# Kernel tuning notes

Measured on AMD Instinct MI355X. Metric: run time of the kernel, lower is better.

The kernel has to match this reference:

```python
import jax, jax.numpy as jnp
import numpy as np

B, L, G, P, K = 16, 2048, 8, 8, 64
CLAMP = 15.0


def _cdist(x, y):
    # Euclidean pairwise distance: x [..., K, 3], y [..., L, 3] -> [..., K, L]
    x2 = jnp.sum(x * x, axis=-1)[..., :, None]
    y2 = jnp.sum(y * y, axis=-1)[..., None, :]
    xy = jnp.einsum('...kc,...lc->...kl', x, y)
    return jnp.sqrt(jnp.maximum(x2 + y2 - 2.0 * xy, 0.0))


def setup_inputs() -> dict:
    key = jax.random.key(0)
    k1, k2, k3 = jax.random.split(key, 3)
    rng = np.random.default_rng(0)
    # each group: K distinct atom indices; each of the P rows is a permutation of them
    auto = np.empty((G, P, K), dtype=np.int64)
    for g in range(G):
        base = rng.permutation(L)[:K]
        auto[g, 0] = base
        for j in range(1, P):
            auto[g, j] = base[rng.permutation(K)]
    return {
        'x_pred': jax.random.normal(k1, (B, L, 3), jnp.float32),
        'x_native': jax.random.normal(k2, (B, L, 3), jnp.float32),
        'x_native_mask': jax.random.randint(k3, (B, L), 0, 2).astype(bool),
        'automorphs': jnp.asarray(auto),
    }


def reference(x_pred, x_native, x_native_mask, automorphs):
    Bn, Ln = x_pred.shape[0], x_pred.shape[1]
    Kn = automorphs.shape[-1]
    batch_idx = jnp.arange(Bn)
    denom = jnp.asarray(Kn * (Ln - Kn), x_pred.dtype)

    def step(carry, a):
        x_nat, nat_mask = carry
        a0 = a[0]                                           # [K]
        # columns NOT in the symmetry group (the ~mask columns)
        colmask = jnp.ones((Ln,), x_pred.dtype).at[a0].set(0.0)
        d_pred = _cdist(x_pred[:, a0], x_pred)              # [B,K,L]
        gath = x_nat[:, a]                                  # [B,P,K,3]
        d_nat = _cdist(gath, x_nat[:, None])                # [B,P,K,L]
        drms = jnp.minimum(jnp.nan_to_num(jnp.square(d_pred[:, None] - d_nat)), CLAMP)
        drms = jnp.sum(drms * colmask, axis=(-1, -2)) / denom   # [B,P] masked mean
        bestj = jnp.argmin(drms, axis=1)                    # first min <=> strict-< update
        sel = gath[batch_idx, bestj]                        # [B,K,3]
        sel_m = nat_mask[:, a][batch_idx, bestj]            # [B,K]
        x_nat = x_nat.at[:, a0].set(sel)
        nat_mask = nat_mask.at[:, a0].set(sel_m)
        return (x_nat, nat_mask), None

    (x_nat, nat_mask), _ = jax.lax.scan(step, (x_native, x_native_mask), automorphs)
    return x_nat, nat_mask
```

## Files before the change

### kernel.cpp

```cpp
#include <hip/hip_runtime.h>
#include <math.h>

#define Bn 16
#define Ln 2048
#define Gn 8
#define Pn 8
#define Kn 64
#define CLAMP_V 15.0f

#define BPB 32
#define NTH 512
#define NWV (NTH / 64)
#define LPB (Ln / BPB)
#define LPW (LPB / NWV)
#define PK  (Pn * Kn)

#define MAGIC(g) (0x5EED0000u | (unsigned)(g))

typedef unsigned long long ull;

__device__ __forceinline__ float wave_sum64(float x) {
#define DPP_ADD(ctrl) \
    x += __int_as_float(__builtin_amdgcn_update_dpp(0, __float_as_int(x), ctrl, 0xf, 0xf, true))
    DPP_ADD(0x111);
    DPP_ADD(0x112);
    DPP_ADD(0x114);
    DPP_ADD(0x118);
    DPP_ADD(0x142);
    DPP_ADD(0x143);
#undef DPP_ADD
    return x;
}

template <int IMM>
__device__ __forceinline__ float swz_xor(float v) {
    return v + __int_as_float(__builtin_amdgcn_ds_swizzle(__float_as_int(v), IMM));
}
__device__ __forceinline__ ull ld_rlx64(const ull* p) {
    return __hip_atomic_load(p, __ATOMIC_RELAXED, __HIP_MEMORY_SCOPE_AGENT);
}
__device__ __forceinline__ void st_rlx64(ull* p, ull v) {
    __hip_atomic_store(p, v, __ATOMIC_RELAXED, __HIP_MEMORY_SCOPE_AGENT);
}

__global__ __launch_bounds__(NTH, 2) void fused_kernel(
    const float* __restrict__ xpred, const float* __restrict__ xnat,
    const int* __restrict__ mask_in, const int* __restrict__ autom,
    float* __restrict__ out_x, float* __restrict__ out_m,
    ull* __restrict__ part) {

    const int tid  = threadIdx.x;
    const int lane = tid & 63;
    const int wv   = tid >> 6;
    const int b    = blockIdx.x >> 5;
    const int c    = blockIdx.x & (BPB - 1);

    __shared__ float4         s_all[Ln];
    __shared__ unsigned short s_idx[Ln];
    __shared__ unsigned char  s_inv[2][Ln];
    __shared__ float4         s_xp[LPB];
    __shared__ float          s_part[NWV][Pn];

    const float* xpb = xpred + (size_t)b * Ln * 3;
    const float* xnb = xnat  + (size_t)b * Ln * 3;

    for (int l = tid; l < Ln; l += NTH) {
        s_idx[l] = (unsigned short)l;
        s_all[l] = make_float4(xnb[l * 3 + 0], xnb[l * 3 + 1], xnb[l * 3 + 2], 0.0f);
    }
    if (wv == 0) {
        const int l = c * LPB + lane;
        s_xp[lane] = make_float4(xpb[l * 3 + 0], xpb[l * 3 + 1], xpb[l * 3 + 2], 0.0f);
    } else if (wv == 2) {
        s_inv[0][autom[lane]] = (unsigned char)lane;
    }
    int   a0k = autom[lane];
    float px = xpb[a0k * 3 + 0], py = xpb[a0k * 3 + 1], pz = xpb[a0k * 3 + 2];
    __syncthreads();

    #pragma unroll 1
    for (int g = 0; g < Gn; g++) {
        const int* ag  = autom + g * PK;
        const int* ag1 = autom + (g + 1) * PK;
        const int  cur = g & 1, nxt = cur ^ 1;
        ull* pg = part + (size_t)(g * Bn + b) * (BPB * Pn);

        const float4 nk = s_all[s_idx[a0k]];
        int sig[Pn];
        #pragma unroll
        for (int p = 0; p < Pn; p++)
            sig[p] = 4 * (int)s_inv[cur][ag[p * Kn + lane]];
        unsigned short jl[LPW];
        #pragma unroll
        for (int i = 0; i < LPW; i++)
            jl[i] = s_idx[c * LPB + wv * LPW + i];

        float acc[Pn];
        #pragma unroll
        for (int p = 0; p < Pn; p++) acc[p] = 0.0f;

        #pragma unroll 2
        for (int i = 0; i < LPW; i++) {
            const int il = wv * LPW + i;
            const int l  = c * LPB + il;
            if (__ballot(a0k == l)) continue;

            const float4 q = s_xp[il];
            const float4 m = s_all[jl[i]];
            const float dx = px - q.x, dy = py - q.y, dz = pz - q.z;
            const float dp = __builtin_amdgcn_sqrtf(dx * dx + dy * dy + dz * dz);
            const float ex = nk.x - m.x, ey = nk.y - m.y, ez = nk.z - m.z;
            const float dn = __builtin_amdgcn_sqrtf(ex * ex + ey * ey + ez * ez);

            #pragma unroll
            for (int p = 0; p < Pn; p++) {
                const float dns = __int_as_float(
                    __builtin_amdgcn_ds_bpermute(sig[p], __float_as_int(dn)));
                const float e = dp - dns;
                acc[p] += fminf(e * e, CLAMP_V);
            }
        }

        #pragma unroll
        for (int p = 0; p < Pn; p++) {
            const float v = wave_sum64(acc[p]);
            if (lane == 63) s_part[wv][p] = v;
        }
        __syncthreads();

        if (wv == 0) {
            float v = s_part[lane >> 3][lane & 7];
            v = swz_xor<0x201F>(v);
            v = swz_xor<0x401F>(v);
            v += __shfl(v, lane + 32, 64);
            if (lane < 8)
                st_rlx64(&pg[c * Pn + lane],
                         ((ull)MAGIC(g) << 32) | (ull)__float_as_uint(v));
        }

        if (g < Gn - 1) {
            a0k = ag1[lane];
            px = xpb[a0k * 3 + 0]; py = xpb[a0k * 3 + 1]; pz = xpb[a0k * 3 + 2];
            if (wv == 2) s_inv[nxt][ag1[lane]] = (unsigned char)lane;
        }

        if (wv == 0) {
            const unsigned magic = MAGIC(g);
            ull q0 = 0, q1 = 0, q2 = 0, q3 = 0;
            bool r0 = false, r1 = false, r2 = false, r3 = false;
            for (;;) {
                if (!r0) { q0 = ld_rlx64(pg + lane);       r0 = (unsigned)(q0 >> 32) == magic; }
                if (!r1) { q1 = ld_rlx64(pg + lane + 64);  r1 = (unsigned)(q1 >> 32) == magic; }
                if (!r2) { q2 = ld_rlx64(pg + lane + 128); r2 = (unsigned)(q2 >> 32) == magic; }
                if (!r3) { q3 = ld_rlx64(pg + lane + 192); r3 = (unsigned)(q3 >> 32) == magic; }
                if (__ballot(!(r0 && r1 && r2 && r3)) == 0ull) break;
                __builtin_amdgcn_s_sleep(1);
            }
            float v = __uint_as_float((unsigned)q0) + __uint_as_float((unsigned)q1)
                    + __uint_as_float((unsigned)q2) + __uint_as_float((unsigned)q3);
            v = swz_xor<0x201F>(v);
            v = swz_xor<0x401F>(v);
            v += __shfl(v, lane + 32, 64);
            float best = __shfl(v, 0, 64);
            int   bj   = 0;
            #pragma unroll
            for (int p = 1; p < Pn; p++) {
                const float t = __shfl(v, p, 64);
                if (t < best) { best = t; bj = p; }
            }
            const unsigned short oldv = s_idx[ag[bj * Kn + lane]];
            s_idx[ag[lane]] = oldv;
        }
        __syncthreads();
    }

    const int l0 = c * LPB;
    if (tid < LPB * 3) {
        const int ll = tid / 3, coord = tid % 3;
        const int l  = l0 + ll;
        const float4 v = s_all[s_idx[l]];
        out_x[((size_t)b * Ln + l) * 3 + coord] =
            (coord == 0) ? v.x : ((coord == 1) ? v.y : v.z);
    } else if (tid < LPB * 4) {
        const int l = l0 + (tid - LPB * 3);
        const int j = s_idx[l];
        out_m[(size_t)b * Ln + l] = (float)mask_in[(size_t)b * Ln + j];
    }
}

extern "C" void kernel_launch(void* const* d_in, const int* in_sizes, int n_in,
                              void* d_out, int out_size, void* d_ws, size_t ws_size,
                              hipStream_t stream) {
    const float* xpred   = (const float*)d_in[0];
    const float* xnat_in = (const float*)d_in[1];
    const int*   mask_in = (const int*)  d_in[2];
    const int*   autom   = (const int*)  d_in[3];

    float* out_x = (float*)d_out;
    float* out_m = out_x + Bn * Ln * 3;

    ull* part = (ull*)d_ws;

    fused_kernel<<<Bn * BPB, NTH, 0, stream>>>(
        xpred, xnat_in, mask_in, autom, out_x, out_m, part);
}
```

Measured before the change: 116.1 us.

## Interleave two batches per block to overlap grid-sync polling with compute

Each block now handles a column slice for two batch items, A and B, and alternates between them. While it polls for batch A's cross-block partial sums, batch B's compute is in flight, and the other way round. This hides the inter-block barrier latency. The column split doubles to 64 blocks per batch, the launch bound rises to 8 blocks per CU, and the full shared-memory copy of native coordinates is dropped in favour of reading coordinates from global memory. The cost is more global or L2 gathers per element and smaller per-block work, and the spin-wait design requires all blocks of a batch to be co-resident.

```diff
diff --git a/kernel.cpp b/kernel.cpp
--- a/kernel.cpp
+++ b/kernel.cpp
@@ -8,7 +8,7 @@
 #define Kn 64
 #define CLAMP_V 15.0f
 
-#define BPB 32
+#define BPB 64
 #define NTH 512
 #define NWV (NTH / 64)
 #define LPB (Ln / BPB)
@@ -43,7 +43,98 @@
     __hip_atomic_store(p, v, __ATOMIC_RELAXED, __HIP_MEMORY_SCOPE_AGENT);
 }
 
-__global__ __launch_bounds__(NTH, 2) void fused_kernel(
+__device__ __forceinline__ void do_cp(
+    int c, int lane, int wv, int a0k, const int* sig,
+    const float4* s_xp, const unsigned short* s_idx, float (*s_part)[Pn],
+    const float* xpb, const float* xnb, ull* pg, unsigned magic) {
+
+    const float px = xpb[a0k * 3 + 0], py = xpb[a0k * 3 + 1], pz = xpb[a0k * 3 + 2];
+    const int   jn = s_idx[a0k];
+    const float nkx = xnb[jn * 3 + 0], nky = xnb[jn * 3 + 1], nkz = xnb[jn * 3 + 2];
+
+    unsigned short jl[LPW];
+    #pragma unroll
+    for (int i = 0; i < LPW; i++) jl[i] = s_idx[c * LPB + wv * LPW + i];
+
+    float acc[Pn];
+    #pragma unroll
+    for (int p = 0; p < Pn; p++) acc[p] = 0.0f;
+
+    #pragma unroll
+    for (int i = 0; i < LPW; i++) {
+        const int il = wv * LPW + i;
+        const int l  = c * LPB + il;
+        if (__ballot(a0k == l)) continue;
+
+        const float4 q = s_xp[il];
+        const int    j = jl[i];
+        const float mx = xnb[j * 3 + 0], my = xnb[j * 3 + 1], mz = xnb[j * 3 + 2];
+
+        const float dx = px - q.x, dy = py - q.y, dz = pz - q.z;
+        const float dp = __builtin_amdgcn_sqrtf(dx * dx + dy * dy + dz * dz);
+        const float ex = nkx - mx, ey = nky - my, ez = nkz - mz;
+        const float dn = __builtin_amdgcn_sqrtf(ex * ex + ey * ey + ez * ez);
+
+        #pragma unroll
+        for (int p = 0; p < Pn; p++) {
+            const float dns = __int_as_float(
+                __builtin_amdgcn_ds_bpermute(sig[p], __float_as_int(dn)));
+            const float e = dp - dns;
+            acc[p] += fminf(e * e, CLAMP_V);
+        }
+    }
+
+    #pragma unroll
+    for (int p = 0; p < Pn; p++) {
+        const float v = wave_sum64(acc[p]);
+        if (lane == 63) s_part[wv][p] = v;
+    }
+    __syncthreads();
+
+    if (wv == 0) {
+        float v = s_part[lane >> 3][lane & 7];
+        v = swz_xor<0x201F>(v);
+        v = swz_xor<0x401F>(v);
+        v += __shfl(v, lane + 32, 64);
+        if (lane < 8)
+            st_rlx64(&pg[c * Pn + lane],
+                     ((ull)magic << 32) | (ull)__float_as_uint(v));
+    }
+}
+
+__device__ __forceinline__ void poll_upd(
+    const int* ag, unsigned short* s_idx, const ull* pg, unsigned magic, int lane) {
+    ull q[8];
+    unsigned rm = 0;
+    for (;;) {
+        #pragma unroll
+        for (int i = 0; i < 8; i++) {
+            if (!(rm & (1u << i))) {
+                q[i] = ld_rlx64(pg + lane + 64 * i);
+                if ((unsigned)(q[i] >> 32) == magic) rm |= 1u << i;
+            }
+        }
+        if (__ballot(rm != 0xFFu) == 0ull) break;
+        __builtin_amdgcn_s_sleep(1);
+    }
+    float v = 0.0f;
+    #pragma unroll
+    for (int i = 0; i < 8; i++) v += __uint_as_float((unsigned)q[i]);
+    v = swz_xor<0x201F>(v);
+    v = swz_xor<0x401F>(v);
+    v += __shfl(v, lane + 32, 64);
+    float best = __shfl(v, 0, 64);
+    int   bj   = 0;
+    #pragma unroll
+    for (int p = 1; p < Pn; p++) {
+        const float t = __shfl(v, p, 64);
+        if (t < best) { best = t; bj = p; }
+    }
+    const unsigned short oldv = s_idx[ag[bj * Kn + lane]];
+    s_idx[ag[lane]] = oldv;
+}
+
+__global__ __launch_bounds__(NTH, 8) void fused_kernel(
     const float* __restrict__ xpred, const float* __restrict__ xnat,
     const int* __restrict__ mask_in, const int* __restrict__ autom,
     float* __restrict__ out_x, float* __restrict__ out_m,
@@ -52,139 +143,95 @@
     const int tid  = threadIdx.x;
     const int lane = tid & 63;
     const int wv   = tid >> 6;
-    const int b    = blockIdx.x >> 5;
+    const int bA   = blockIdx.x >> 6;
+    const int bB   = bA + 8;
     const int c    = blockIdx.x & (BPB - 1);
 
-    __shared__ float4         s_all[Ln];
-    __shared__ unsigned short s_idx[Ln];
+    __shared__ unsigned short s_idxA[Ln];
+    __shared__ unsigned short s_idxB[Ln];
     __shared__ unsigned char  s_inv[2][Ln];
-    __shared__ float4         s_xp[LPB];
+    __shared__ float4         s_xpA[LPB];
+    __shared__ float4         s_xpB[LPB];
     __shared__ float          s_part[NWV][Pn];
 
-    const float* xpb = xpred + (size_t)b * Ln * 3;
-    const float* xnb = xnat  + (size_t)b * Ln * 3;
+    const float* xpA = xpred + (size_t)bA * Ln * 3;
+    const float* xpB = xpred + (size_t)bB * Ln * 3;
+    const float* xnA = xnat  + (size_t)bA * Ln * 3;
+    const float* xnB = xnat  + (size_t)bB * Ln * 3;
 
     for (int l = tid; l < Ln; l += NTH) {
-        s_idx[l] = (unsigned short)l;
-        s_all[l] = make_float4(xnb[l * 3 + 0], xnb[l * 3 + 1], xnb[l * 3 + 2], 0.0f);
+        s_idxA[l] = (unsigned short)l;
+        s_idxB[l] = (unsigned short)l;
     }
     if (wv == 0) {
-        const int l = c * LPB + lane;
-        s_xp[lane] = make_float4(xpb[l * 3 + 0], xpb[l * 3 + 1], xpb[l * 3 + 2], 0.0f);
+        const int half = lane >> 5, col = lane & 31;
+        const int l = c * LPB + col;
+        const float* xp = half ? xpB : xpA;
+        const float4 v = make_float4(xp[l * 3 + 0], xp[l * 3 + 1], xp[l * 3 + 2], 0.0f);
+        if (half) s_xpB[col] = v; else s_xpA[col] = v;
     } else if (wv == 2) {
         s_inv[0][autom[lane]] = (unsigned char)lane;
     }
-    int   a0k = autom[lane];
-    float px = xpb[a0k * 3 + 0], py = xpb[a0k * 3 + 1], pz = xpb[a0k * 3 + 2];
     __syncthreads();
+
+    int a0k = autom[lane];
+    int sig[Pn];
+    #pragma unroll
+    for (int p = 0; p < Pn; p++) sig[p] = 4 * (int)s_inv[0][autom[p * Kn + lane]];
+
+    do_cp(c, lane, wv, a0k, sig, s_xpA, s_idxA, s_part, xpA, xnA,
+          part + (size_t)(0 * Bn + bA) * BPB * Pn, MAGIC(0));
+    __syncthreads();
+    do_cp(c, lane, wv, a0k, sig, s_xpB, s_idxB, s_part, xpB, xnB,
+          part + (size_t)(0 * Bn + bB) * BPB * Pn, MAGIC(0));
 
     #pragma unroll 1
     for (int g = 0; g < Gn; g++) {
+        const bool hn  = (g < Gn - 1);
         const int* ag  = autom + g * PK;
         const int* ag1 = autom + (g + 1) * PK;
-        const int  cur = g & 1, nxt = cur ^ 1;
-        ull* pg = part + (size_t)(g * Bn + b) * (BPB * Pn);
-
-        const float4 nk = s_all[s_idx[a0k]];
-        int sig[Pn];
-        #pragma unroll
-        for (int p = 0; p < Pn; p++)
-            sig[p] = 4 * (int)s_inv[cur][ag[p * Kn + lane]];
-        unsigned short jl[LPW];
-        #pragma unroll
-        for (int i = 0; i < LPW; i++)
-            jl[i] = s_idx[c * LPB + wv * LPW + i];
-
-        float acc[Pn];
-        #pragma unroll
-        for (int p = 0; p < Pn; p++) acc[p] = 0.0f;
-
-        #pragma unroll 2
-        for (int i = 0; i < LPW; i++) {
-            const int il = wv * LPW + i;
-            const int l  = c * LPB + il;
-            if (__ballot(a0k == l)) continue;
-
-            const float4 q = s_xp[il];
-            const float4 m = s_all[jl[i]];
-            const float dx = px - q.x, dy = py - q.y, dz = pz - q.z;
-            const float dp = __builtin_amdgcn_sqrtf(dx * dx + dy * dy + dz * dz);
-            const float ex = nk.x - m.x, ey = nk.y - m.y, ez = nk.z - m.z;
-            const float dn = __builtin_amdgcn_sqrtf(ex * ex + ey * ey + ez * ez);
-
+
+        if (wv == 0)
+            poll_upd(ag, s_idxA, part + (size_t)(g * Bn + bA) * BPB * Pn,
+                     MAGIC(g), lane);
+        if (hn && wv == 2)
+            s_inv[(g + 1) & 1][ag1[lane]] = (unsigned char)lane;
+        __syncthreads();
+
+        if (hn) {
             #pragma unroll
-            for (int p = 0; p < Pn; p++) {
-                const float dns = __int_as_float(
-                    __builtin_amdgcn_ds_bpermute(sig[p], __float_as_int(dn)));
-                const float e = dp - dns;
-                acc[p] += fminf(e * e, CLAMP_V);
-            }
-        }
-
-        #pragma unroll
-        for (int p = 0; p < Pn; p++) {
-            const float v = wave_sum64(acc[p]);
-            if (lane == 63) s_part[wv][p] = v;
-        }
+            for (int p = 0; p < Pn; p++)
+                sig[p] = 4 * (int)s_inv[(g + 1) & 1][ag1[p * Kn + lane]];
+            a0k = ag1[lane];
+            do_cp(c, lane, wv, a0k, sig, s_xpA, s_idxA, s_part, xpA, xnA,
+                  part + (size_t)((g + 1) * Bn + bA) * BPB * Pn, MAGIC(g + 1));
+        }
+
+        if (wv == 0)
+            poll_upd(ag, s_idxB, part + (size_t)(g * Bn + bB) * BPB * Pn,
+                     MAGIC(g), lane);
         __syncthreads();
 
-        if (wv == 0) {
-            float v = s_part[lane >> 3][lane & 7];
-            v = swz_xor<0x201F>(v);
-            v = swz_xor<0x401F>(v);
-            v += __shfl(v, lane + 32, 64);
-            if (lane < 8)
-                st_rlx64(&pg[c * Pn + lane],
-                         ((ull)MAGIC(g) << 32) | (ull)__float_as_uint(v));
-        }
-
-        if (g < Gn - 1) {
-            a0k = ag1[lane];
-            px = xpb[a0k * 3 + 0]; py = xpb[a0k * 3 + 1]; pz = xpb[a0k * 3 + 2];
-            if (wv == 2) s_inv[nxt][ag1[lane]] = (unsigned char)lane;
-        }
-
-        if (wv == 0) {
-            const unsigned magic = MAGIC(g);
-            ull q0 = 0, q1 = 0, q2 = 0, q3 = 0;
-            bool r0 = false, r1 = false, r2 = false, r3 = false;
-            for (;;) {
-                if (!r0) { q0 = ld_rlx64(pg + lane);       r0 = (unsigned)(q0 >> 32) == magic; }
-                if (!r1) { q1 = ld_rlx64(pg + lane + 64);  r1 = (unsigned)(q1 >> 32) == magic; }
-                if (!r2) { q2 = ld_rlx64(pg + lane + 128); r2 = (unsigned)(q2 >> 32) == magic; }
-                if (!r3) { q3 = ld_rlx64(pg + lane + 192); r3 = (unsigned)(q3 >> 32) == magic; }
-                if (__ballot(!(r0 && r1 && r2 && r3)) == 0ull) break;
-                __builtin_amdgcn_s_sleep(1);
-            }
-            float v = __uint_as_float((unsigned)q0) + __uint_as_float((unsigned)q1)
-                    + __uint_as_float((unsigned)q2) + __uint_as_float((unsigned)q3);
-            v = swz_xor<0x201F>(v);
-            v = swz_xor<0x401F>(v);
-            v += __shfl(v, lane + 32, 64);
-            float best = __shfl(v, 0, 64);
-            int   bj   = 0;
-            #pragma unroll
-            for (int p = 1; p < Pn; p++) {
-                const float t = __shfl(v, p, 64);
-                if (t < best) { best = t; bj = p; }
-            }
-            const unsigned short oldv = s_idx[ag[bj * Kn + lane]];
-            s_idx[ag[lane]] = oldv;
-        }
-        __syncthreads();
-    }
-
-    const int l0 = c * LPB;
-    if (tid < LPB * 3) {
-        const int ll = tid / 3, coord = tid % 3;
+        if (hn) {
+            do_cp(c, lane, wv, a0k, sig, s_xpB, s_idxB, s_part, xpB, xnB,
+                  part + (size_t)((g + 1) * Bn + bB) * BPB * Pn, MAGIC(g + 1));
+        }
+    }
+
+    const int t = tid & 255;
+    const unsigned short* si = (tid < 256) ? s_idxA : s_idxB;
+    const float* xn = (tid < 256) ? xnA : xnB;
+    const int    bo = (tid < 256) ? bA : bB;
+    const int    l0 = c * LPB;
+    if (t < LPB * 3) {
+        const int ll = t / 3, coord = t % 3;
         const int l  = l0 + ll;
-        const float4 v = s_all[s_idx[l]];
-        out_x[((size_t)b * Ln + l) * 3 + coord] =
-            (coord == 0) ? v.x : ((coord == 1) ? v.y : v.z);
-    } else if (tid < LPB * 4) {
-        const int l = l0 + (tid - LPB * 3);
-        const int j = s_idx[l];
-        out_m[(size_t)b * Ln + l] = (float)mask_in[(size_t)b * Ln + j];
+        const int j  = si[l];
+        out_x[((size_t)bo * Ln + l) * 3 + coord] = xn[j * 3 + coord];
+    } else if (t < LPB * 4) {
+        const int l = l0 + (t - LPB * 3);
+        const int j = si[l];
+        out_m[(size_t)bo * Ln + l] = (float)mask_in[(size_t)bo * Ln + j];
     }
 }
 
@@ -201,6 +248,6 @@
 
     ull* part = (ull*)d_ws;
 
-    fused_kernel<<<Bn * BPB, NTH, 0, stream>>>(
+    fused_kernel<<<8 * BPB, NTH, 0, stream>>>(
         xpred, xnat_in, mask_in, autom, out_x, out_m, part);
 }
```

Measured after the change: 155.2 us. 33.7% more time.

## Drop shared coordinate cache, read natives from global, speculatively prefetch next-group indices

Applied to the files above, without the earlier changes.

Removes the 32KB shared float4 copy of the native coordinates and reads them directly from global or L2. This shrinks LDS enough to raise the launch bound to 6 blocks per CU. Every s_inv table is built up front, and the per-wave partial reduction now uses an LDS atomic counter, so the last wave does the reduce instead of waiting at a block barrier. Next-group indices and coordinates are prefetched before the grid-wide wait and patched afterwards using per-column update stamps. The cost is more global loads in the inner loop and extra bookkeeping.

```diff
diff --git a/kernel.cpp b/kernel.cpp
--- a/kernel.cpp
+++ b/kernel.cpp
@@ -43,7 +43,7 @@
     __hip_atomic_store(p, v, __ATOMIC_RELAXED, __HIP_MEMORY_SCOPE_AGENT);
 }
 
-__global__ __launch_bounds__(NTH, 2) void fused_kernel(
+__global__ __launch_bounds__(NTH, 6) void fused_kernel(
     const float* __restrict__ xpred, const float* __restrict__ xnat,
     const int* __restrict__ mask_in, const int* __restrict__ autom,
     float* __restrict__ out_x, float* __restrict__ out_m,
@@ -55,45 +55,45 @@
     const int b    = blockIdx.x >> 5;
     const int c    = blockIdx.x & (BPB - 1);
 
-    __shared__ float4         s_all[Ln];
     __shared__ unsigned short s_idx[Ln];
-    __shared__ unsigned char  s_inv[2][Ln];
+    __shared__ signed char    s_stamp[Ln];
+    __shared__ unsigned char  s_inv[Gn][Ln];
     __shared__ float4         s_xp[LPB];
     __shared__ float          s_part[NWV][Pn];
+    __shared__ int            s_cnt;
 
     const float* xpb = xpred + (size_t)b * Ln * 3;
     const float* xnb = xnat  + (size_t)b * Ln * 3;
 
     for (int l = tid; l < Ln; l += NTH) {
-        s_idx[l] = (unsigned short)l;
-        s_all[l] = make_float4(xnb[l * 3 + 0], xnb[l * 3 + 1], xnb[l * 3 + 2], 0.0f);
-    }
+        s_idx[l]   = (unsigned short)l;
+        s_stamp[l] = -1;
+    }
+    s_inv[wv][autom[wv * PK + lane]] = (unsigned char)lane;
     if (wv == 0) {
         const int l = c * LPB + lane;
         s_xp[lane] = make_float4(xpb[l * 3 + 0], xpb[l * 3 + 1], xpb[l * 3 + 2], 0.0f);
-    } else if (wv == 2) {
-        s_inv[0][autom[lane]] = (unsigned char)lane;
-    }
+    }
+    if (tid == 0) s_cnt = 0;
+
     int   a0k = autom[lane];
     float px = xpb[a0k * 3 + 0], py = xpb[a0k * 3 + 1], pz = xpb[a0k * 3 + 2];
+    float nkx = xnb[a0k * 3 + 0], nky = xnb[a0k * 3 + 1], nkz = xnb[a0k * 3 + 2];
+    unsigned short jl[LPW];
+    #pragma unroll
+    for (int i = 0; i < LPW; i++) jl[i] = (unsigned short)(c * LPB + wv * LPW + i);
     __syncthreads();
+
+    int sig[Pn];
+    #pragma unroll
+    for (int p = 0; p < Pn; p++) sig[p] = 4 * (int)s_inv[0][autom[p * Kn + lane]];
 
     #pragma unroll 1
     for (int g = 0; g < Gn; g++) {
+        const bool hn  = (g < Gn - 1);
         const int* ag  = autom + g * PK;
-        const int* ag1 = autom + (g + 1) * PK;
-        const int  cur = g & 1, nxt = cur ^ 1;
+        const int* ag1 = ag + PK;
         ull* pg = part + (size_t)(g * Bn + b) * (BPB * Pn);
-
-        const float4 nk = s_all[s_idx[a0k]];
-        int sig[Pn];
-        #pragma unroll
-        for (int p = 0; p < Pn; p++)
-            sig[p] = 4 * (int)s_inv[cur][ag[p * Kn + lane]];
-        unsigned short jl[LPW];
-        #pragma unroll
-        for (int i = 0; i < LPW; i++)
-            jl[i] = s_idx[c * LPB + wv * LPW + i];
 
         float acc[Pn];
         #pragma unroll
@@ -106,10 +106,12 @@
             if (__ballot(a0k == l)) continue;
 
             const float4 q = s_xp[il];
-            const float4 m = s_all[jl[i]];
+            const int    j = jl[i];
+            const float mx = xnb[j * 3 + 0], my = xnb[j * 3 + 1], mz = xnb[j * 3 + 2];
+
             const float dx = px - q.x, dy = py - q.y, dz = pz - q.z;
             const float dp = __builtin_amdgcn_sqrtf(dx * dx + dy * dy + dz * dz);
-            const float ex = nk.x - m.x, ey = nk.y - m.y, ez = nk.z - m.z;
+            const float ex = nkx - mx, ey = nky - my, ez = nkz - mz;
             const float dn = __builtin_amdgcn_sqrtf(ex * ex + ey * ey + ez * ez);
 
             #pragma unroll
@@ -126,9 +128,12 @@
             const float v = wave_sum64(acc[p]);
             if (lane == 63) s_part[wv][p] = v;
         }
-        __syncthreads();
-
-        if (wv == 0) {
+        int old = 0;
+        if (lane == 63)
+            old = __hip_atomic_fetch_add(&s_cnt, 1, __ATOMIC_ACQ_REL,
+                                         __HIP_MEMORY_SCOPE_WORKGROUP);
+        old = __shfl(old, 63, 64);
+        if (old == NWV - 1) {
             float v = s_part[lane >> 3][lane & 7];
             v = swz_xor<0x201F>(v);
             v = swz_xor<0x401F>(v);
@@ -136,12 +141,19 @@
             if (lane < 8)
                 st_rlx64(&pg[c * Pn + lane],
                          ((ull)MAGIC(g) << 32) | (ull)__float_as_uint(v));
-        }
-
-        if (g < Gn - 1) {
-            a0k = ag1[lane];
-            px = xpb[a0k * 3 + 0]; py = xpb[a0k * 3 + 1]; pz = xpb[a0k * 3 + 2];
-            if (wv == 2) s_inv[nxt][ag1[lane]] = (unsigned char)lane;
+            if (lane == 0) s_cnt = 0;
+        }
+
+        int   a0k1 = 0;
+        float px1 = 0, py1 = 0, pz1 = 0, nk1x = 0, nk1y = 0, nk1z = 0;
+        unsigned short jl1[LPW];
+        if (hn) {
+            a0k1 = ag1[lane];
+            px1 = xpb[a0k1 * 3 + 0]; py1 = xpb[a0k1 * 3 + 1]; pz1 = xpb[a0k1 * 3 + 2];
+            const int jn = s_idx[a0k1];
+            nk1x = xnb[jn * 3 + 0]; nk1y = xnb[jn * 3 + 1]; nk1z = xnb[jn * 3 + 2];
+            #pragma unroll
+            for (int i = 0; i < LPW; i++) jl1[i] = s_idx[c * LPB + wv * LPW + i];
         }
 
         if (wv == 0) {
@@ -169,18 +181,36 @@
                 if (t < best) { best = t; bj = p; }
             }
             const unsigned short oldv = s_idx[ag[bj * Kn + lane]];
-            s_idx[ag[lane]] = oldv;
+            s_idx[ag[lane]]   = oldv;
+            s_stamp[ag[lane]] = (signed char)g;
         }
         __syncthreads();
+
+        if (hn) {
+            if (s_stamp[a0k1] == (signed char)g) {
+                const int jn = s_idx[a0k1];
+                nk1x = xnb[jn * 3 + 0]; nk1y = xnb[jn * 3 + 1]; nk1z = xnb[jn * 3 + 2];
+            }
+            #pragma unroll
+            for (int i = 0; i < LPW; i++) {
+                const int col = c * LPB + wv * LPW + i;
+                if (s_stamp[col] == (signed char)g) jl1[i] = s_idx[col];
+                jl[i] = jl1[i];
+            }
+            a0k = a0k1; px = px1; py = py1; pz = pz1;
+            nkx = nk1x; nky = nk1y; nkz = nk1z;
+            #pragma unroll
+            for (int p = 0; p < Pn; p++)
+                sig[p] = 4 * (int)s_inv[g + 1][ag1[p * Kn + lane]];
+        }
     }
 
     const int l0 = c * LPB;
     if (tid < LPB * 3) {
         const int ll = tid / 3, coord = tid % 3;
         const int l  = l0 + ll;
-        const float4 v = s_all[s_idx[l]];
-        out_x[((size_t)b * Ln + l) * 3 + coord] =
-            (coord == 0) ? v.x : ((coord == 1) ? v.y : v.z);
+        const int j  = s_idx[l];
+        out_x[((size_t)b * Ln + l) * 3 + coord] = xnb[j * 3 + coord];
     } else if (tid < LPB * 4) {
         const int l = l0 + (tid - LPB * 3);
         const int j = s_idx[l];
```

Result: slower. 124.2 us (+7.0%).
